# Kernel tuning notes

Measured on AMD Instinct MI355X. Metric: run time of the kernel, lower is better.

The kernel has to match this reference:

```python
import jax, jax.numpy as jnp
import numpy as np

EPS = 1.1920929e-07  # torch.finfo(float32).eps (nn.RMSNorm default eps=None)
ROPE_BASE = 10000.0


def _rmsnorm(x, g):
    # x: (..., d). torch nn.RMSNorm: x * rsqrt(mean(x^2) + eps) * g
    var = jnp.mean(jnp.square(x), axis=-1, keepdims=True)
    return x * jax.lax.rsqrt(var + EPS) * g


def _rope(x):
    # x: (b, h, s, d). Matches RotaryPositionEmbedding: half-split concat layout.
    s, d = x.shape[2], x.shape[3]
    pos = jnp.arange(s, dtype=x.dtype)[:, None]                      # (s,1)
    freqs = ROPE_BASE ** (-jnp.arange(0, d, 2, dtype=x.dtype) / d)   # (d/2,)
    ang = pos * freqs                                                # (s, d/2)
    c, sn = jnp.cos(ang), jnp.sin(ang)
    xe, xo = x[..., ::2], x[..., 1::2]
    return jnp.concatenate([xe * c - xo * sn, xe * sn + xo * c], axis=-1)


def setup_inputs() -> dict:
    key = jax.random.key(0)
    ks = jax.random.split(key, 9)
    B, S, D, F = 1, 2048, 4096, 11008
    W = 0.02  # weight scale to keep activations sane
    return {
        "x": jax.random.normal(ks[0], (B, S, D), jnp.float32),
        "wq": jax.random.normal(ks[1], (D, D), jnp.float32) * W,
        "wk": jax.random.normal(ks[2], (D, D), jnp.float32) * W,
        "wv": jax.random.normal(ks[3], (D, D), jnp.float32) * W,
        "wo": jax.random.normal(ks[4], (D, D), jnp.float32) * W,
        "w1": jax.random.normal(ks[5], (D, F), jnp.float32) * W,
        "w2": jax.random.normal(ks[6], (F, D), jnp.float32) * W,
        "w3": jax.random.normal(ks[7], (D, F), jnp.float32) * W,
        "g_attn": jnp.ones((D,), jnp.float32),
        "g_ffn": jnp.ones((D,), jnp.float32),
    }


def reference(x, wq, wk, wv, wo, w1, w2, w3, g_attn, g_ffn):
    n_heads = 32
    bsz, seqlen, dim = x.shape
    head_dim = dim // n_heads

    h = _rmsnorm(x, g_attn)
    # (b,s,d) @ (d,d) -> (b,s,h,hd) -> (b,h,s,hd)
    xq = (h @ wq).reshape(bsz, seqlen, n_heads, head_dim).transpose(0, 2, 1, 3)
    xk = (h @ wk).reshape(bsz, seqlen, n_heads, head_dim).transpose(0, 2, 1, 3)
    xv = (h @ wv).reshape(bsz, seqlen, n_heads, head_dim).transpose(0, 2, 1, 3)

    xq = _rope(xq)
    xk = _rope(xk)

    # NOTE: faithful to source: NO 1/sqrt(head_dim) scaling, NO causal mask.
    scores = jnp.einsum("bhqd,bhkd->bhqk", xq, xk)
    scores = jax.nn.softmax(scores, axis=-1)
    out = jnp.einsum("bhqk,bhkd->bhqd", scores, xv)        # (b,h,s,hd)
    out = out.transpose(0, 2, 1, 3).reshape(bsz, seqlen, dim)
    xo = out @ wo

    # NOTE: faithful to source: no residual connections; silu on w3 branch.
    h2 = _rmsnorm(xo, g_ffn)
    x1 = h2 @ w1
    x3 = jax.nn.silu(h2 @ w3)
    return (x1 * x3) @ w2
```

## Files before the change

### kernel.cpp

```cpp
#include <hip/hip_runtime.h>
#include <math.h>

typedef unsigned short u16;
typedef short short8 __attribute__((ext_vector_type(8)));
typedef float f32x4 __attribute__((ext_vector_type(4)));

#define DEV static __device__ __forceinline__

DEV float bf2f(u16 h) { union { unsigned int u; float f; } v; v.u = ((unsigned int)h) << 16; return v.f; }
DEV u16 f2bf(float f) {
  union { float f; unsigned int u; } v; v.f = f;
  unsigned int r = v.u + 0x7FFFu + ((v.u >> 16) & 1u);
  return (u16)(r >> 16);
}

DEV void gl_lds16(const void* g, void* l) {
  __builtin_amdgcn_global_load_lds(
      (const __attribute__((address_space(1))) unsigned int*)g,
      (__attribute__((address_space(3))) unsigned int*)l, 16, 0, 0);
}

template <int N> DEV void vm_wait() {
  if constexpr (N == 0) asm volatile("s_waitcnt vmcnt(0)" ::: "memory");
  else if constexpr (N == 6) asm volatile("s_waitcnt vmcnt(6)" ::: "memory");
  else if constexpr (N == 8) asm volatile("s_waitcnt vmcnt(8)" ::: "memory");
  else static_assert(N == 0 || N == 6 || N == 8, "add literal");
}

DEV void lgkm0_pin() {
  asm volatile("s_waitcnt lgkmcnt(0)" ::: "memory");
  __builtin_amdgcn_sched_barrier(0);
}

DEV void xcd_swizzle(int& bx, int& by) {
  int gx = gridDim.x, gy = gridDim.y;
  int lin = by * gx + bx;
  int xcd = lin & 7, i = lin >> 3;
  if ((gx & 7) == 0) {
    int cx = gx >> 3;
    bx = xcd * cx + i % cx;
    by = i / cx;
  } else {
    int cpx = (gx * gy) >> 3;
    int swz = xcd * cpx + i;
    bx = swz % gx;
    by = swz / gx;
  }
}

template <bool SPLIT>
__global__ __launch_bounds__(256) void rmsnorm_kernel(
    const float* __restrict__ x, const float* __restrict__ g,
    u16* __restrict__ oh, u16* __restrict__ ol) {
  int row = blockIdx.x, t = threadIdx.x;
  const float* xr = x + (size_t)row * 4096;
  float4 vals[4];
  float s = 0.f;
#pragma unroll
  for (int i = 0; i < 4; i++) {
    vals[i] = ((const float4*)xr)[t + i * 256];
    s += vals[i].x * vals[i].x + vals[i].y * vals[i].y + vals[i].z * vals[i].z + vals[i].w * vals[i].w;
  }
#pragma unroll
  for (int m = 1; m < 64; m <<= 1) s += __shfl_xor(s, m);
  __shared__ float red[4];
  if ((t & 63) == 0) red[t >> 6] = s;
  __syncthreads();
  s = red[0] + red[1] + red[2] + red[3];
  float rinv = rsqrtf(s * (1.f / 4096.f) + 1.1920929e-07f);
#pragma unroll
  for (int i = 0; i < 4; i++) {
    float4 gv = ((const float4*)g)[t + i * 256];
    float4 v = vals[i];
    float f[4] = {v.x * rinv * gv.x, v.y * rinv * gv.y, v.z * rinv * gv.z, v.w * rinv * gv.w};
    ushort4 rh, rl;
    u16* hp = (u16*)&rh; u16* lp = (u16*)&rl;
#pragma unroll
    for (int j = 0; j < 4; j++) {
      u16 hi = f2bf(f[j]);
      hp[j] = hi;
      if (SPLIT) lp[j] = f2bf(f[j] - bf2f(hi));
    }
    ((ushort4*)(oh + (size_t)row * 4096))[t + i * 256] = rh;
    if (SPLIT) ((ushort4*)(ol + (size_t)row * 4096))[t + i * 256] = rl;
  }
}

__global__ void tconv_kernel(const float* __restrict__ in, u16* __restrict__ out, int K, int N) {
  __shared__ float tile[64][65];
  int k0 = blockIdx.y * 64, n0 = blockIdx.x * 64;
  int tx = threadIdx.x, ty = threadIdx.y;
#pragma unroll
  for (int i = 0; i < 8; i++) {
    int r = ty + 8 * i;
    float2 v = *(const float2*)&in[(size_t)(k0 + r) * N + n0 + tx * 2];
    tile[r][tx * 2] = v.x;
    tile[r][tx * 2 + 1] = v.y;
  }
  __syncthreads();
#pragma unroll
  for (int i = 0; i < 8; i++) {
    int c = ty + 8 * i;
    ushort2 o;
    o.x = f2bf(tile[tx * 2][c]);
    o.y = f2bf(tile[tx * 2 + 1][c]);
    *(ushort2*)&out[(size_t)(n0 + c) * K + k0 + tx * 2] = o;
  }
}

__global__ void tconv_ilv_kernel(const float* __restrict__ in, u16* __restrict__ out,
                                 int K, int N, int off) {
  __shared__ float tile[64][65];
  int k0 = blockIdx.y * 64, n0 = blockIdx.x * 64;
  int tx = threadIdx.x, ty = threadIdx.y;
#pragma unroll
  for (int i = 0; i < 8; i++) {
    int r = ty + 8 * i;
    float2 v = *(const float2*)&in[(size_t)(k0 + r) * N + n0 + tx * 2];
    tile[r][tx * 2] = v.x;
    tile[r][tx * 2 + 1] = v.y;
  }
  __syncthreads();
#pragma unroll
  for (int i = 0; i < 8; i++) {
    int c = ty + 8 * i;
    int n = n0 + c;
    int orow = ((n >> 7) << 8) + (n & 127) + off;
    ushort2 o;
    o.x = f2bf(tile[tx * 2][c]);
    o.y = f2bf(tile[tx * 2 + 1][c]);
    *(ushort2*)&out[(size_t)orow * K + k0 + tx * 2] = o;
  }
}

__global__ void tconv_split_kernel(const float* __restrict__ in, u16* __restrict__ oh,
                                   u16* __restrict__ ol, int K, int N) {
  __shared__ float tile[64][65];
  int k0 = blockIdx.y * 64, n0 = blockIdx.x * 64;
  int tx = threadIdx.x, ty = threadIdx.y;
#pragma unroll
  for (int i = 0; i < 8; i++) {
    int r = ty + 8 * i;
    float2 v = *(const float2*)&in[(size_t)(k0 + r) * N + n0 + tx * 2];
    tile[r][tx * 2] = v.x;
    tile[r][tx * 2 + 1] = v.y;
  }
  __syncthreads();
#pragma unroll
  for (int i = 0; i < 8; i++) {
    int c = ty + 8 * i;
    float f0 = tile[tx * 2][c], f1 = tile[tx * 2 + 1][c];
    u16 h0 = f2bf(f0), h1 = f2bf(f1);
    ushort2 vh, vl;
    vh.x = h0; vh.y = h1;
    vl.x = f2bf(f0 - bf2f(h0)); vl.y = f2bf(f1 - bf2f(h1));
    size_t idx = (size_t)(n0 + c) * K + k0 + tx * 2;
    *(ushort2*)&oh[idx] = vh;
    *(ushort2*)&ol[idx] = vl;
  }
}

__global__ __launch_bounds__(256) void rope_table_kernel(float* __restrict__ tab) {
  int i = blockIdx.x * 256 + threadIdx.x;
  int j = i & 63, s = i >> 6;
  double freq = pow(10000.0, -(double)j / 64.0);
  double ang = (double)s * freq;
  tab[i * 2] = (float)cos(ang);
  tab[i * 2 + 1] = (float)sin(ang);
}

__global__ __launch_bounds__(256) void rope_inplace_kernel(
    u16* hi, u16* lo, const float* __restrict__ tab) {
  int idx = blockIdx.x * 256 + threadIdx.x;
  int j = idx & 63, hd = (idx >> 6) & 63, s = idx >> 12;
  size_t base = (size_t)s * 8192 + hd * 128;
  float xe = bf2f(hi[base + 2 * j]) + bf2f(lo[base + 2 * j]);
  float xo = bf2f(hi[base + 2 * j + 1]) + bf2f(lo[base + 2 * j + 1]);
  float cs = tab[(s * 64 + j) * 2], sn = tab[(s * 64 + j) * 2 + 1];
  float r0 = xe * cs - xo * sn;
  float r1 = xe * sn + xo * cs;
  u16 h0 = f2bf(r0), h1 = f2bf(r1);
  hi[base + j] = h0;      lo[base + j] = f2bf(r0 - bf2f(h0));
  hi[base + 64 + j] = h1; lo[base + 64 + j] = f2bf(r1 - bf2f(h1));
}

template <int OUT, bool TRIK>
__global__ __launch_bounds__(512, 2) void gemm8_kernel(
    const u16* __restrict__ A, const u16* __restrict__ A2,
    const u16* __restrict__ B, const u16* __restrict__ B2,
    void* __restrict__ C, u16* __restrict__ C2,
    int M, int N, int K, int lda, int ldb) {
  __shared__ __attribute__((aligned(16))) u16 SMEM[65536];
  int t = threadIdx.x, l = t & 63, w = t >> 6;
  int bx = blockIdx.x, by = blockIdx.y;
  xcd_swizzle(bx, by);
  int m0 = by * 256, n0 = bx * 256;
  int wm = w >> 2, wn = w & 3, bh = wn >> 1;
  f32x4 acc[8][4] = {};
  int nk = K >> 6;

  auto AsP = [&](int d, int h) -> u16* { return SMEM + (d * 2 + h) * 8192; };
  auto BsP = [&](int d, int h) -> u16* { return SMEM + 32768 + (d * 2 + h) * 8192; };

  auto stageA = [&](int kt, int dd) {
    const u16* Ab = A; int kc = kt << 6;
    if (TRIK) { int seg = kt >> 6; Ab = (seg == 1) ? A2 : A; kc = (kt & 63) << 6; }
#pragma unroll
    for (int i = 0; i < 4; i++) {
      int id = i * 512 + t;
      int hh = id >> 10, idc = id & 1023;
      int r = idc >> 3, cb = idc & 7;
      int csw = ((cb * 16) ^ ((r & 7) << 4)) >> 1;
      gl_lds16(&Ab[(size_t)(m0 + hh * 128 + r) * lda + kc + csw], AsP(dd, hh) + idc * 8);
    }
  };
  auto stageB = [&](int kt, int dd) {
    const u16* Bb = B; int kc = kt << 6;
    if (TRIK) { int seg = kt >> 6; Bb = (seg == 2) ? B2 : B; kc = (kt & 63) << 6; }
#pragma unroll
    for (int i = 0; i < 4; i++) {
      int id = i * 512 + t;
      int hh = id >> 10, idc = id & 1023;
      int r = idc >> 3, cb = idc & 7;
      int csw = ((cb * 16) ^ ((r & 7) << 4)) >> 1;
      gl_lds16(&Bb[(size_t)(n0 + hh * 128 + r) * ldb + kc + csw], BsP(dd, hh) + idc * 8);
    }
  };

  int lq = l >> 4, lr = l & 15;
  short8 af[4][2], bf[4][2];
  auto rdA = [&](int d, int mh) {
    const char* Ax = (const char*)AsP(d, wm);
#pragma unroll
    for (int m = 0; m < 4; m++) {
      int r = mh * 64 + m * 16 + lr;
      int rb = r * 128, rx = (r & 7) << 4;
#pragma unroll
      for (int kh = 0; kh < 2; kh++)
        af[m][kh] = *(const short8*)(Ax + rb + ((kh * 64 + lq * 16) ^ rx));
    }
  };
  auto rdB2 = [&](int d, int nlo, int nhi) {
    const char* Bx = (const char*)BsP(d, bh);
#pragma unroll
    for (int n = 0; n < 4; n++) {
      if (n < nlo || n >= nhi) continue;
      int r = (wn & 1) * 64 + n * 16 + lr;
      int rb = r * 128, rx = (r & 7) << 4;
#pragma unroll
      for (int kh = 0; kh < 2; kh++)
        bf[n][kh] = *(const short8*)(Bx + rb + ((kh * 64 + lq * 16) ^ rx));
    }
  };
  auto mm8 = [&](int mo, int no) {
    __builtin_amdgcn_s_setprio(1);
#pragma unroll
    for (int m = 0; m < 4; m++)
#pragma unroll
      for (int n = 0; n < 2; n++)
#pragma unroll
        for (int kh = 0; kh < 2; kh++)
          acc[mo + m][no + n] =
              __builtin_amdgcn_mfma_f32_16x16x32_bf16(af[m][kh], bf[no + n][kh], acc[mo + m][no + n], 0, 0, 0);
    __builtin_amdgcn_s_setprio(0);
  };

  stageB(0, 0); stageA(0, 0);
  stageB(1, 1); stageA(1, 1);
  vm_wait<8>();
  __builtin_amdgcn_s_barrier();

  for (int kt = 0; kt < nk; ++kt) {
    int d = kt & 1;
    rdA(d, 0);
    rdB2(d, 0, 2);
    __builtin_amdgcn_s_barrier();
    lgkm0_pin();
    mm8(0, 0);
    __builtin_amdgcn_s_barrier();
    rdB2(d, 2, 4);
    __builtin_amdgcn_s_barrier();
    lgkm0_pin();
    mm8(0, 2);
    __builtin_amdgcn_s_barrier();
    rdA(d, 1);
    if (kt + 2 < nk) stageB(kt + 2, d);
    __builtin_amdgcn_s_barrier();
    lgkm0_pin();
    mm8(4, 2);
    __builtin_amdgcn_s_barrier();
    if (kt + 2 < nk) stageA(kt + 2, d);
    __builtin_amdgcn_s_barrier();
    mm8(4, 0);
    if (kt + 2 < nk) vm_wait<8>();
    else vm_wait<0>();
    __builtin_amdgcn_s_barrier();
  }

  if (OUT == 3) {
    __syncthreads();
    float* EPI = (float*)SMEM;
    if (wn >= 2) {
#pragma unroll
      for (int m = 0; m < 8; m++)
#pragma unroll
        for (int i = 0; i < 4; i++) {
          int rl = wm * 128 + m * 16 + lq * 4 + i;
#pragma unroll
          for (int n = 0; n < 4; n++)
            EPI[rl * 128 + (wn - 2) * 64 + n * 16 + lr] = acc[m][n][i];
        }
    }
    __syncthreads();
    if (wn < 2) {
      u16* Ob = (u16*)C;
      int cb = n0 >> 1;
#pragma unroll
      for (int m = 0; m < 8; m++)
#pragma unroll
        for (int i = 0; i < 4; i++) {
          int rl = wm * 128 + m * 16 + lq * 4 + i;
          int row = m0 + rl;
#pragma unroll
          for (int n = 0; n < 4; n++) {
            float a = acc[m][n][i];
            float b = EPI[rl * 128 + wn * 64 + n * 16 + lr];
            float r = a * (b / (1.f + expf(-b)));
            Ob[(size_t)row * N + cb + wn * 64 + n * 16 + lr] = f2bf(r);
          }
        }
    }
    return;
  }

#pragma unroll
  for (int m = 0; m < 8; m++) {
#pragma unroll
    for (int i = 0; i < 4; i++) {
      int row = m0 + wm * 128 + m * 16 + lq * 4 + i;
      size_t rb = (size_t)row * N + n0 + wn * 64 + lr;
#pragma unroll
      for (int n = 0; n < 4; n++) {
        float f = acc[m][n][i];
        if (OUT == 0) ((float*)C)[rb + n * 16] = f;
        else if (OUT == 1) ((u16*)C)[rb + n * 16] = f2bf(f);
        else {
          u16 hi = f2bf(f);
          ((u16*)C)[rb + n * 16] = hi;
          C2[rb + n * 16] = f2bf(f - bf2f(hi));
        }
      }
    }
  }
}

template <int OUT>
__global__ __launch_bounds__(512, 2) void gemm8n_kernel(
    const u16* __restrict__ A, const u16* __restrict__ B, void* __restrict__ C,
    int M, int N, int K, int lda, int ldb) {
  __shared__ __attribute__((aligned(16))) u16 As[2][128 * 64];
  __shared__ __attribute__((aligned(16))) u16 Bs3[3][256 * 64];
  int t = threadIdx.x, l = t & 63, w = t >> 6;
  int bx = blockIdx.x, by = blockIdx.y;
  xcd_swizzle(bx, by);
  int m0 = by * 128, n0 = bx * 256;
  int wm = w >> 2, wn = w & 3;
  f32x4 acc[4][4] = {};
  int nk = K >> 6;

  auto stageA = [&](int kt, int dd) {
    int kc = kt << 6;
#pragma unroll
    for (int i = 0; i < 2; i++) {
      int id = i * 512 + t;
      int r = id >> 3, cb = id & 7;
      int csw = ((cb * 16) ^ ((r & 7) << 4)) >> 1;
      gl_lds16(&A[(size_t)(m0 + r) * lda + kc + csw], &As[dd][id * 8]);
    }
  };
  auto stageB = [&](int kt, int bb) {
    int kc = kt << 6;
#pragma unroll
    for (int i = 0; i < 4; i++) {
      int id = i * 512 + t;
      int r = id >> 3, cb = id & 7;
      int csw = ((cb * 16) ^ ((r & 7) << 4)) >> 1;
      gl_lds16(&B[(size_t)(n0 + r) * ldb + kc + csw], &Bs3[bb][id * 8]);
    }
  };

  int lq = l >> 4, lr = l & 15;
  short8 af0[4], af1[4], bf0[4], bf1[4];
  auto rdA4 = [&](short8 (&dst)[4], int d, int kh) {
    const char* Ax = (const char*)As[d];
#pragma unroll
    for (int m = 0; m < 4; m++) {
      int r = wm * 64 + m * 16 + lr;
      dst[m] = *(const short8*)(Ax + r * 128 + ((kh * 64 + lq * 16) ^ ((r & 7) << 4)));
    }
  };
  auto rdB4 = [&](short8 (&dst)[4], int bb, int kh) {
    const char* Bx = (const char*)Bs3[bb];
#pragma unroll
    for (int n = 0; n < 4; n++) {
      int r = wn * 64 + n * 16 + lr;
      dst[n] = *(const short8*)(Bx + r * 128 + ((kh * 64 + lq * 16) ^ ((r & 7) << 4)));
    }
  };
  auto mm16 = [&](short8 (&a)[4], short8 (&b)[4]) {
    __builtin_amdgcn_s_setprio(1);
#pragma unroll
    for (int m = 0; m < 4; m++)
#pragma unroll
      for (int n = 0; n < 4; n++)
        acc[m][n] = __builtin_amdgcn_mfma_f32_16x16x32_bf16(a[m], b[n], acc[m][n], 0, 0, 0);
    __builtin_amdgcn_s_setprio(0);
  };

  stageB(0, 0); stageA(0, 0);
  stageB(1, 1); stageA(1, 1);
  vm_wait<6>();
  __builtin_amdgcn_s_barrier();

  for (int kt = 0; kt < nk; ++kt) {
    int d = kt & 1;
    int bb = kt % 3, bb2 = (kt + 2) % 3;
    if (kt + 2 < nk) stageB(kt + 2, bb2);
    rdA4(af0, d, 0); rdB4(bf0, bb, 0);
    __builtin_amdgcn_s_barrier();
    lgkm0_pin();
    mm16(af0, bf0);
    __builtin_amdgcn_s_barrier();
    rdA4(af1, d, 1); rdB4(bf1, bb, 1);
    lgkm0_pin();
    __builtin_amdgcn_s_barrier();
    if (kt + 2 < nk) { stageA(kt + 2, d); vm_wait<6>(); }
    else vm_wait<0>();
    mm16(af1, bf1);
    __builtin_amdgcn_s_barrier();
  }
  if (OUT == 2) {
    u16* Cb = (u16*)C;
#pragma unroll
    for (int m = 0; m < 4; m++) {
      int sbase = m0 + wm * 64 + m * 16 + lq * 4;
#pragma unroll
      for (int n = 0; n < 4; n++) {
        int dg = n0 + wn * 64 + n * 16 + lr;
        ushort4 pk;
        pk.x = f2bf(acc[m][n][0]); pk.y = f2bf(acc[m][n][1]);
        pk.z = f2bf(acc[m][n][2]); pk.w = f2bf(acc[m][n][3]);
        *(ushort4*)&Cb[(size_t)dg * M + sbase] = pk;
      }
    }
    return;
  }
#pragma unroll
  for (int m = 0; m < 4; m++) {
#pragma unroll
    for (int i = 0; i < 4; i++) {
      int row = m0 + wm * 64 + m * 16 + lq * 4 + i;
      size_t rb = (size_t)row * N + n0 + wn * 64 + lr;
#pragma unroll
      for (int n = 0; n < 4; n++) {
        float f = acc[m][n][i];
        if (OUT == 0) ((float*)C)[rb + n * 16] = f;
        else ((u16*)C)[rb + n * 16] = f2bf(f);
      }
    }
  }
}

__global__ __launch_bounds__(256) void attn_kernel(
    const u16* __restrict__ qh, const u16* __restrict__ ql,
    const u16* __restrict__ kh, const u16* __restrict__ kl,
    const u16* __restrict__ vt, u16* __restrict__ out) {
  const int QS = 8192;
  __shared__ __attribute__((aligned(16))) u16 KH[64 * 128];
  __shared__ __attribute__((aligned(16))) u16 KL[64 * 128];
  __shared__ __attribute__((aligned(16))) u16 Vl[128 * 64];
  __shared__ __attribute__((aligned(16))) u16 Pl[4][16 * 72];
  int t = threadIdx.x, l = t & 63, w = t >> 6;
  int hd = blockIdx.y, q0 = blockIdx.x * 64;
  int qrow = q0 + w * 16 + (l & 15);
  size_t qoff = (size_t)qrow * QS + hd * 128 + (l >> 4) * 8;
  short8 qfh[4], qfl[4];
#pragma unroll
  for (int kc = 0; kc < 4; kc++) {
    qfh[kc] = *(const short8*)&qh[qoff + kc * 32];
    qfl[kc] = *(const short8*)&ql[qoff + kc * 32];
  }
  f32x4 accO[8] = {};
  float mrun = -__builtin_inff(), lrun = 0.f;
  for (int kv0 = 0; kv0 < 2048; kv0 += 64) {
#pragma unroll
    for (int i = 0; i < 4; i++) {
      int ci = i * 256 + t;
      int row = ci >> 4;
      int cb = (ci & 15) ^ (row & 7);
      size_t src = (size_t)(kv0 + row) * QS + hd * 128 + cb * 8;
      gl_lds16(&kh[src], &KH[ci * 8]);
      gl_lds16(&kl[src], &KL[ci * 8]);
    }
#pragma unroll
    for (int i = 0; i < 4; i++) {
      int ci = i * 256 + t;
      int row = ci >> 3;
      int cb = (ci & 7) ^ (row & 7);
      gl_lds16(&vt[((size_t)hd * 128 + row) * 2048 + kv0 + cb * 8], &Vl[ci * 8]);
    }
    __syncthreads();
    f32x4 accS[4];
#pragma unroll
    for (int mm = 0; mm < 4; mm++) {
      accS[mm] = (f32x4){0.f, 0.f, 0.f, 0.f};
#pragma unroll
      for (int kc = 0; kc < 4; kc++) {
        int rowk = mm * 16 + (l & 15);
        int logb = rowk * 256 + kc * 64 + (l >> 4) * 16;
        int phys = logb ^ ((rowk & 7) << 4);
        short8 a_h = *(const short8*)((const char*)KH + phys);
        short8 a_l = *(const short8*)((const char*)KL + phys);
        accS[mm] = __builtin_amdgcn_mfma_f32_16x16x32_bf16(a_h, qfh[kc], accS[mm], 0, 0, 0);
        accS[mm] = __builtin_amdgcn_mfma_f32_16x16x32_bf16(a_h, qfl[kc], accS[mm], 0, 0, 0);
        accS[mm] = __builtin_amdgcn_mfma_f32_16x16x32_bf16(a_l, qfh[kc], accS[mm], 0, 0, 0);
      }
    }
    float tmax = -__builtin_inff();
#pragma unroll
    for (int mm = 0; mm < 4; mm++)
      tmax = fmaxf(tmax, fmaxf(fmaxf(accS[mm][0], accS[mm][1]), fmaxf(accS[mm][2], accS[mm][3])));
    tmax = fmaxf(tmax, __shfl_xor(tmax, 16));
    tmax = fmaxf(tmax, __shfl_xor(tmax, 32));
    float mnew = fmaxf(mrun, tmax);
    float scale = expf(mrun - mnew);
    float psum = 0.f;
#pragma unroll
    for (int mm = 0; mm < 4; mm++) {
      float p0 = expf(accS[mm][0] - mnew), p1 = expf(accS[mm][1] - mnew);
      float p2 = expf(accS[mm][2] - mnew), p3 = expf(accS[mm][3] - mnew);
      psum += (p0 + p1) + (p2 + p3);
      ushort4 pk;
      pk.x = f2bf(p0); pk.y = f2bf(p1); pk.z = f2bf(p2); pk.w = f2bf(p3);
      *(ushort4*)&Pl[w][(l & 15) * 72 + mm * 16 + (l >> 4) * 4] = pk;
    }
    psum += __shfl_xor(psum, 16);
    psum += __shfl_xor(psum, 32);
    lrun = lrun * scale + psum;
    mrun = mnew;
#pragma unroll
    for (int mm = 0; mm < 8; mm++) accO[mm] = accO[mm] * scale;
#pragma unroll
    for (int kc2 = 0; kc2 < 2; kc2++) {
      short8 bp = *(const short8*)((const char*)&Pl[w][0] + (l & 15) * 144 + kc2 * 64 + (l >> 4) * 16);
#pragma unroll
      for (int mm = 0; mm < 8; mm++) {
        int rowd = mm * 16 + (l & 15);
        int logb = rowd * 128 + kc2 * 64 + (l >> 4) * 16;
        int phys = logb ^ ((rowd & 7) << 4);
        short8 av = *(const short8*)((const char*)Vl + phys);
        accO[mm] = __builtin_amdgcn_mfma_f32_16x16x32_bf16(av, bp, accO[mm], 0, 0, 0);
      }
    }
    __syncthreads();
  }
  float rinv = 1.f / lrun;
#pragma unroll
  for (int mm = 0; mm < 8; mm++) {
    ushort4 pk;
    pk.x = f2bf(accO[mm][0] * rinv); pk.y = f2bf(accO[mm][1] * rinv);
    pk.z = f2bf(accO[mm][2] * rinv); pk.w = f2bf(accO[mm][3] * rinv);
    *(ushort4*)&out[(size_t)qrow * 4096 + hd * 128 + mm * 16 + (l >> 4) * 4] = pk;
  }
}

extern "C" void kernel_launch(void* const* d_in, const int* in_sizes, int n_in,
                              void* d_out, int out_size, void* d_ws, size_t ws_size,
                              hipStream_t stream) {
  const float* x      = (const float*)d_in[0];
  const float* wq     = (const float*)d_in[1];
  const float* wk     = (const float*)d_in[2];
  const float* wv     = (const float*)d_in[3];
  const float* wo     = (const float*)d_in[4];
  const float* w1     = (const float*)d_in[5];
  const float* w2     = (const float*)d_in[6];
  const float* w3     = (const float*)d_in[7];
  const float* g_attn = (const float*)d_in[8];
  const float* g_ffn  = (const float*)d_in[9];

  char* ws = (char*)d_ws;
  char* R0 = ws;
  char* R1 = R0 + (size_t)22016 * 4096 * 2;
  char* R2 = R1 + (size_t)8192 * 4096 * 2;
  char* R3 = R2 + (size_t)2 * 2048 * 4096 * 2;
  char* R4 = R3 + (size_t)2 * 2048 * 8192 * 2;
  char* RT = R4 + (size_t)2 * 2048 * 4096 * 2;
  (void)ws_size; (void)in_sizes; (void)n_in; (void)out_size;

  u16* wA     = (u16*)R0;
  u16* wB     = (u16*)R1;
  u16* h_hi   = (u16*)R2;
  u16* h_lo   = (u16*)(R2 + (size_t)2048 * 4096 * 2);
  u16* qk_hi  = (u16*)R3;
  u16* qk_lo  = (u16*)(R3 + (size_t)2048 * 8192 * 2);
  u16* ao     = (u16*)R4;
  u16* vT     = (u16*)(R4 + (size_t)2048 * 4096 * 2);
  float* xo   = (float*)R1;
  u16* h2     = (u16*)(R1 + (size_t)2048 * 4096 * 4);
  u16* x1silu = (u16*)R3;
  float* tab  = (float*)RT;

  dim3 tb(32, 8);

  rope_table_kernel<<<512, 256, 0, stream>>>(tab);
  rmsnorm_kernel<true><<<2048, 256, 0, stream>>>(x, g_attn, h_hi, h_lo);
  tconv_split_kernel<<<dim3(64, 64), tb, 0, stream>>>(wq, wA, wB, 4096, 4096);
  tconv_split_kernel<<<dim3(64, 64), tb, 0, stream>>>(wk, wA + (size_t)4096 * 4096, wB + (size_t)4096 * 4096, 4096, 4096);
  gemm8_kernel<2, true><<<dim3(32, 8), 512, 0, stream>>>(
      h_hi, h_lo, wA, wB, qk_hi, qk_lo, 2048, 8192, 12288, 4096, 4096);
  rope_inplace_kernel<<<32768, 256, 0, stream>>>(qk_hi, qk_lo, tab);
  tconv_kernel<<<dim3(64, 64), tb, 0, stream>>>(wv, wA, 4096, 4096);
  gemm8n_kernel<2><<<dim3(16, 16), 512, 0, stream>>>(h_hi, wA, vT, 2048, 4096, 4096, 4096, 4096);
  attn_kernel<<<dim3(32, 32), 256, 0, stream>>>(qk_hi, qk_lo, qk_hi + 4096, qk_lo + 4096, vT, ao);
  tconv_kernel<<<dim3(64, 64), tb, 0, stream>>>(wo, wA, 4096, 4096);
  gemm8n_kernel<0><<<dim3(16, 16), 512, 0, stream>>>(ao, wA, xo, 2048, 4096, 4096, 4096, 4096);
  rmsnorm_kernel<false><<<2048, 256, 0, stream>>>(xo, g_ffn, h2, nullptr);
  tconv_ilv_kernel<<<dim3(172, 64), tb, 0, stream>>>(w1, wA, 4096, 11008, 0);
  tconv_ilv_kernel<<<dim3(172, 64), tb, 0, stream>>>(w3, wA, 4096, 11008, 128);
  gemm8_kernel<3, false><<<dim3(86, 8), 512, 0, stream>>>(
      h2, nullptr, wA, nullptr, x1silu, nullptr, 2048, 11008, 4096, 4096, 4096);
  tconv_kernel<<<dim3(64, 172), tb, 0, stream>>>(w2, wA, 11008, 4096);
  gemm8n_kernel<0><<<dim3(16, 16), 512, 0, stream>>>(x1silu, wA, (float*)d_out, 2048, 4096, 11008, 11008, 11008);
}
```

Before: 1.668 ms.

## Process two query row-groups per wave in attention to reuse K/V tiles

Each attention block now covers 128 query rows instead of 64, so every wave handles two 16-row query groups against each K/V tile it loads into LDS. This halves the total K/V global-to-LDS traffic and the number of blocks (grid drops from 32x32 to 16x32). The cost is roughly double the per-wave register state (Q fragments, output accumulators), which the launch bound of 2 blocks per SM may make tight. It also leaves 512 blocks, which could lower occupancy and latency hiding.

```diff
diff --git a/kernel.cpp b/kernel.cpp
--- a/kernel.cpp
+++ b/kernel.cpp
@@ -471,7 +471,7 @@
   }
 }
 
-__global__ __launch_bounds__(256) void attn_kernel(
+__global__ __launch_bounds__(256, 2) void attn_kernel(
     const u16* __restrict__ qh, const u16* __restrict__ ql,
     const u16* __restrict__ kh, const u16* __restrict__ kl,
     const u16* __restrict__ vt, u16* __restrict__ out) {
@@ -479,19 +479,25 @@
   __shared__ __attribute__((aligned(16))) u16 KH[64 * 128];
   __shared__ __attribute__((aligned(16))) u16 KL[64 * 128];
   __shared__ __attribute__((aligned(16))) u16 Vl[128 * 64];
-  __shared__ __attribute__((aligned(16))) u16 Pl[4][16 * 72];
+  __shared__ __attribute__((aligned(16))) u16 Pl[8][16 * 72];
   int t = threadIdx.x, l = t & 63, w = t >> 6;
-  int hd = blockIdx.y, q0 = blockIdx.x * 64;
-  int qrow = q0 + w * 16 + (l & 15);
-  size_t qoff = (size_t)qrow * QS + hd * 128 + (l >> 4) * 8;
-  short8 qfh[4], qfl[4];
-#pragma unroll
-  for (int kc = 0; kc < 4; kc++) {
-    qfh[kc] = *(const short8*)&qh[qoff + kc * 32];
-    qfl[kc] = *(const short8*)&ql[qoff + kc * 32];
-  }
-  f32x4 accO[8] = {};
-  float mrun = -__builtin_inff(), lrun = 0.f;
+  int hd = blockIdx.y, q0 = blockIdx.x * 128;
+  int lr = l & 15, lq = l >> 4;
+  int qrow0 = q0 + (w * 2) * 16 + lr;
+  int qrow1 = q0 + (w * 2 + 1) * 16 + lr;
+  short8 qfh[2][4], qfl[2][4];
+#pragma unroll
+  for (int g = 0; g < 2; g++) {
+    size_t qoff = (size_t)(g ? qrow1 : qrow0) * QS + hd * 128 + lq * 8;
+#pragma unroll
+    for (int kc = 0; kc < 4; kc++) {
+      qfh[g][kc] = *(const short8*)&qh[qoff + kc * 32];
+      qfl[g][kc] = *(const short8*)&ql[qoff + kc * 32];
+    }
+  }
+  f32x4 accO[2][8] = {};
+  float mrun[2] = {-__builtin_inff(), -__builtin_inff()};
+  float lrun[2] = {0.f, 0.f};
   for (int kv0 = 0; kv0 < 2048; kv0 += 64) {
 #pragma unroll
     for (int i = 0; i < 4; i++) {
@@ -510,67 +516,75 @@
       gl_lds16(&vt[((size_t)hd * 128 + row) * 2048 + kv0 + cb * 8], &Vl[ci * 8]);
     }
     __syncthreads();
-    f32x4 accS[4];
-#pragma unroll
-    for (int mm = 0; mm < 4; mm++) {
-      accS[mm] = (f32x4){0.f, 0.f, 0.f, 0.f};
-#pragma unroll
-      for (int kc = 0; kc < 4; kc++) {
-        int rowk = mm * 16 + (l & 15);
-        int logb = rowk * 256 + kc * 64 + (l >> 4) * 16;
-        int phys = logb ^ ((rowk & 7) << 4);
-        short8 a_h = *(const short8*)((const char*)KH + phys);
-        short8 a_l = *(const short8*)((const char*)KL + phys);
-        accS[mm] = __builtin_amdgcn_mfma_f32_16x16x32_bf16(a_h, qfh[kc], accS[mm], 0, 0, 0);
-        accS[mm] = __builtin_amdgcn_mfma_f32_16x16x32_bf16(a_h, qfl[kc], accS[mm], 0, 0, 0);
-        accS[mm] = __builtin_amdgcn_mfma_f32_16x16x32_bf16(a_l, qfh[kc], accS[mm], 0, 0, 0);
+#pragma unroll
+    for (int g = 0; g < 2; g++) {
+      f32x4 accS[4];
+#pragma unroll
+      for (int mm = 0; mm < 4; mm++) {
+        accS[mm] = (f32x4){0.f, 0.f, 0.f, 0.f};
+#pragma unroll
+        for (int kc = 0; kc < 4; kc++) {
+          int rowk = mm * 16 + lr;
+          int logb = rowk * 256 + kc * 64 + lq * 16;
+          int phys = logb ^ ((rowk & 7) << 4);
+          short8 a_h = *(const short8*)((const char*)KH + phys);
+          short8 a_l = *(const short8*)((const char*)KL + phys);
+          accS[mm] = __builtin_amdgcn_mfma_f32_16x16x32_bf16(a_h, qfh[g][kc], accS[mm], 0, 0, 0);
+          accS[mm] = __builtin_amdgcn_mfma_f32_16x16x32_bf16(a_h, qfl[g][kc], accS[mm], 0, 0, 0);
+          accS[mm] = __builtin_amdgcn_mfma_f32_16x16x32_bf16(a_l, qfh[g][kc], accS[mm], 0, 0, 0);
+        }
       }
-    }
-    float tmax = -__builtin_inff();
-#pragma unroll
-    for (int mm = 0; mm < 4; mm++)
-      tmax = fmaxf(tmax, fmaxf(fmaxf(accS[mm][0], accS[mm][1]), fmaxf(accS[mm][2], accS[mm][3])));
-    tmax = fmaxf(tmax, __shfl_xor(tmax, 16));
-    tmax = fmaxf(tmax, __shfl_xor(tmax, 32));
-    float mnew = fmaxf(mrun, tmax);
-    float scale = expf(mrun - mnew);
-    float psum = 0.f;
-#pragma unroll
-    for (int mm = 0; mm < 4; mm++) {
-      float p0 = expf(accS[mm][0] - mnew), p1 = expf(accS[mm][1] - mnew);
-      float p2 = expf(accS[mm][2] - mnew), p3 = expf(accS[mm][3] - mnew);
-      psum += (p0 + p1) + (p2 + p3);
+      float tmax = -__builtin_inff();
+#pragma unroll
+      for (int mm = 0; mm < 4; mm++)
+        tmax = fmaxf(tmax, fmaxf(fmaxf(accS[mm][0], accS[mm][1]), fmaxf(accS[mm][2], accS[mm][3])));
+      tmax = fmaxf(tmax, __shfl_xor(tmax, 16));
+      tmax = fmaxf(tmax, __shfl_xor(tmax, 32));
+      float mnew = fmaxf(mrun[g], tmax);
+      float scale = expf(mrun[g] - mnew);
+      float psum = 0.f;
+      u16* Pw = &Pl[w * 2 + g][0];
+#pragma unroll
+      for (int mm = 0; mm < 4; mm++) {
+        float p0 = expf(accS[mm][0] - mnew), p1 = expf(accS[mm][1] - mnew);
+        float p2 = expf(accS[mm][2] - mnew), p3 = expf(accS[mm][3] - mnew);
+        psum += (p0 + p1) + (p2 + p3);
+        ushort4 pk;
+        pk.x = f2bf(p0); pk.y = f2bf(p1); pk.z = f2bf(p2); pk.w = f2bf(p3);
+        *(ushort4*)&Pw[lr * 72 + mm * 16 + lq * 4] = pk;
+      }
+      psum += __shfl_xor(psum, 16);
+      psum += __shfl_xor(psum, 32);
+      lrun[g] = lrun[g] * scale + psum;
+      mrun[g] = mnew;
+#pragma unroll
+      for (int mm = 0; mm < 8; mm++) accO[g][mm] = accO[g][mm] * scale;
+#pragma unroll
+      for (int kc2 = 0; kc2 < 2; kc2++) {
+        short8 bp = *(const short8*)((const char*)Pw + lr * 144 + kc2 * 64 + lq * 16);
+#pragma unroll
+        for (int mm = 0; mm < 8; mm++) {
+          int rowd = mm * 16 + lr;
+          int logb = rowd * 128 + kc2 * 64 + lq * 16;
+          int phys = logb ^ ((rowd & 7) << 4);
+          short8 av = *(const short8*)((const char*)Vl + phys);
+          accO[g][mm] = __builtin_amdgcn_mfma_f32_16x16x32_bf16(av, bp, accO[g][mm], 0, 0, 0);
+        }
+      }
+    }
+    __syncthreads();
+  }
+#pragma unroll
+  for (int g = 0; g < 2; g++) {
+    float rinv = 1.f / lrun[g];
+    int qrow = g ? qrow1 : qrow0;
+#pragma unroll
+    for (int mm = 0; mm < 8; mm++) {
       ushort4 pk;
-      pk.x = f2bf(p0); pk.y = f2bf(p1); pk.z = f2bf(p2); pk.w = f2bf(p3);
-      *(ushort4*)&Pl[w][(l & 15) * 72 + mm * 16 + (l >> 4) * 4] = pk;
-    }
-    psum += __shfl_xor(psum, 16);
-    psum += __shfl_xor(psum, 32);
-    lrun = lrun * scale + psum;
-    mrun = mnew;
-#pragma unroll
-    for (int mm = 0; mm < 8; mm++) accO[mm] = accO[mm] * scale;
-#pragma unroll
-    for (int kc2 = 0; kc2 < 2; kc2++) {
-      short8 bp = *(const short8*)((const char*)&Pl[w][0] + (l & 15) * 144 + kc2 * 64 + (l >> 4) * 16);
-#pragma unroll
-      for (int mm = 0; mm < 8; mm++) {
-        int rowd = mm * 16 + (l & 15);
-        int logb = rowd * 128 + kc2 * 64 + (l >> 4) * 16;
-        int phys = logb ^ ((rowd & 7) << 4);
-        short8 av = *(const short8*)((const char*)Vl + phys);
-        accO[mm] = __builtin_amdgcn_mfma_f32_16x16x32_bf16(av, bp, accO[mm], 0, 0, 0);
-      }
-    }
-    __syncthreads();
-  }
-  float rinv = 1.f / lrun;
-#pragma unroll
-  for (int mm = 0; mm < 8; mm++) {
-    ushort4 pk;
-    pk.x = f2bf(accO[mm][0] * rinv); pk.y = f2bf(accO[mm][1] * rinv);
-    pk.z = f2bf(accO[mm][2] * rinv); pk.w = f2bf(accO[mm][3] * rinv);
-    *(ushort4*)&out[(size_t)qrow * 4096 + hd * 128 + mm * 16 + (l >> 4) * 4] = pk;
+      pk.x = f2bf(accO[g][mm][0] * rinv); pk.y = f2bf(accO[g][mm][1] * rinv);
+      pk.z = f2bf(accO[g][mm][2] * rinv); pk.w = f2bf(accO[g][mm][3] * rinv);
+      *(ushort4*)&out[(size_t)qrow * 4096 + hd * 128 + mm * 16 + lq * 4] = pk;
+    }
   }
 }
 
@@ -621,7 +635,7 @@
   rope_inplace_kernel<<<32768, 256, 0, stream>>>(qk_hi, qk_lo, tab);
   tconv_kernel<<<dim3(64, 64), tb, 0, stream>>>(wv, wA, 4096, 4096);
   gemm8n_kernel<2><<<dim3(16, 16), 512, 0, stream>>>(h_hi, wA, vT, 2048, 4096, 4096, 4096, 4096);
-  attn_kernel<<<dim3(32, 32), 256, 0, stream>>>(qk_hi, qk_lo, qk_hi + 4096, qk_lo + 4096, vT, ao);
+  attn_kernel<<<dim3(16, 32), 256, 0, stream>>>(qk_hi, qk_lo, qk_hi + 4096, qk_lo + 4096, vT, ao);
   tconv_kernel<<<dim3(64, 64), tb, 0, stream>>>(wo, wA, 4096, 4096);
   gemm8n_kernel<0><<<dim3(16, 16), 512, 0, stream>>>(ao, wA, xo, 2048, 4096, 4096, 4096, 4096);
   rmsnorm_kernel<false><<<2048, 256, 0, stream>>>(xo, g_ffn, h2, nullptr);
```

After: 1.675 ms. Within noise of the previous version (+0.4%).
